# Performance work log

Hardware: AMD Instinct MI355X
Metric: run time of the kernel (lower is better)

## Reference

```python
import jax, jax.numpy as jnp
import numpy as np

N = 50000      # nodes
E = 800000     # edges (before self-loops)
IN = 128       # in_channels
C = 64         # hidden_channels
HD = 4         # heads
SLOPE = 0.2    # GATConv leaky_relu negative slope
EPS_BN = 1e-5


def add_self_loops(edge_index, n):
    loop = jnp.arange(n, dtype=edge_index.dtype)
    return jnp.concatenate([edge_index, jnp.stack([loop, loop])], axis=1)


def gat_conv(x, edge_index, W, a_src, a_dst, bias, heads, out_c, concat, n):
    src, dst = edge_index[0], edge_index[1]
    h = (x @ W).reshape(n, heads, out_c)                 # [N,H,C]
    al_s = jnp.sum(h * a_src, axis=-1)                   # [N,H]
    al_d = jnp.sum(h * a_dst, axis=-1)                   # [N,H]
    e = jax.nn.leaky_relu(al_s[src] + al_d[dst], SLOPE)  # [Etot,H]
    m = jax.ops.segment_max(e, dst, num_segments=n)      # segment softmax (stable)
    ex = jnp.exp(e - m[dst])
    s = jax.ops.segment_sum(ex, dst, num_segments=n)
    alpha = ex / (s[dst] + 1e-16)                        # [Etot,H]
    out = jax.ops.segment_sum(h[src] * alpha[:, :, None], dst, num_segments=n)
    out = out.reshape(n, heads * out_c) if concat else out.mean(axis=1)
    return out + bias


def batch_norm(x, gamma, beta):
    mu = x.mean(axis=0)
    var = x.var(axis=0)
    return (x - mu) * jax.lax.rsqrt(var + EPS_BN) * gamma + beta


def setup_inputs() -> dict:
    key = jax.random.key(0)
    ks = jax.random.split(key, 24)
    f = lambda k, shp, sc: (jax.random.normal(k, shp, dtype=jnp.float32) * sc)
    HC = HD * C
    return {
        "x": f(ks[0], (N, IN), 1.0),
        "edge_index": jax.random.randint(ks[1], (2, E), 0, N, dtype=jnp.int64),
        # conv1: IN -> C, heads=HD, concat
        "W1": f(ks[2], (IN, HC), 0.05), "as1": f(ks[3], (HD, C), 0.05),
        "ad1": f(ks[4], (HD, C), 0.05), "b1": f(ks[5], (HC,), 0.02),
        "g1": jnp.ones((HC,), jnp.float32), "bb1": jnp.zeros((HC,), jnp.float32),
        # conv2: HC -> C, heads=HD, concat
        "W2": f(ks[6], (HC, HC), 0.05), "as2": f(ks[7], (HD, C), 0.05),
        "ad2": f(ks[8], (HD, C), 0.05), "b2": f(ks[9], (HC,), 0.02),
        "g2": jnp.ones((HC,), jnp.float32), "bb2": jnp.zeros((HC,), jnp.float32),
        # conv3: HC -> C, heads=1, mean
        "W3": f(ks[10], (HC, C), 0.05), "as3": f(ks[11], (1, C), 0.05),
        "ad3": f(ks[12], (1, C), 0.05), "b3": f(ks[13], (C,), 0.02),
        # skips
        "Ws1": f(ks[14], (IN, HC), 0.05), "bs1": f(ks[15], (HC,), 0.02),
        "Ws2": f(ks[16], (HC, C), 0.05), "bs2": f(ks[17], (C,), 0.02),
    }


def reference(x, edge_index, W1, as1, ad1, b1, g1, bb1,
              W2, as2, ad2, b2, g2, bb2,
              W3, as3, ad3, b3, Ws1, bs1, Ws2, bs2):
    ei = add_self_loops(edge_index, N)
    x_init = x @ Ws1 + bs1
    h = gat_conv(x, ei, W1, as1, ad1, b1, HD, C, True, N)
    h = jax.nn.elu(batch_norm(h, g1, bb1)) + x_init
    x_skip = h @ Ws2 + bs2
    h = gat_conv(h, ei, W2, as2, ad2, b2, HD, C, True, N)
    h = jax.nn.elu(batch_norm(h, g2, bb2))
    out = gat_conv(h, ei, W3, as3, ad3, b3, 1, C, False, N) + x_skip
    return out
```

## Files before the change

kernel.cpp:

```cpp
#include <hip/hip_runtime.h>
#include <hip/hip_bf16.h>
#include <cstdint>
#include <cstddef>


#define LRELU_SLOPE 0.2f
#define NSTATB 256

typedef __attribute__((ext_vector_type(8))) short short8;
typedef __attribute__((ext_vector_type(4))) float f32x4;

__device__ __forceinline__ float bf2f(unsigned short u) {
  union { unsigned int i; float f; } t; t.i = ((unsigned int)u) << 16; return t.f;
}
__device__ __forceinline__ unsigned short f2bf(float f) {
  __hip_bfloat16 h = __float2bfloat16(f);
  return *reinterpret_cast<unsigned short*>(&h);
}

template<int K, int WAVES_GAT, int WAVES_SKIP>
__global__ __launch_bounds__((WAVES_GAT + WAVES_SKIP) * 64)
void gemm_gat_fused(const unsigned short* __restrict__ A,
                    const unsigned short* __restrict__ BtH,
                    const unsigned short* __restrict__ BtS,
                    const float* __restrict__ a_s, const float* __restrict__ a_d,
                    const float* __restrict__ biasS,
                    unsigned short* __restrict__ Hout,
                    float* __restrict__ als, float* __restrict__ ald,
                    unsigned short* __restrict__ Sout, int M) {
  constexpr int NKS = K / 32;
  constexpr int NH  = WAVES_GAT * 64;
  constexpr int NS  = WAVES_SKIP * 64;
  const int wid  = threadIdx.x >> 6;
  const int lane = threadIdx.x & 63;
  const int r    = lane & 15;
  const int q    = lane >> 4;
  const int koff = q * 8;
  const bool isGat = wid < WAVES_GAT;
  const int colbase = isGat ? wid * 64 : (wid - WAVES_GAT) * 64;
  const unsigned short* Bt = isGat ? BtH : BtS;

  short8 b[4][NKS];
  #pragma unroll
  for (int nf = 0; nf < 4; ++nf)
    #pragma unroll
    for (int ks = 0; ks < NKS; ++ks)
      b[nf][ks] = *(const short8*)(Bt + (size_t)(colbase + nf * 16 + r) * K + ks * 32 + koff);

  float as4[4] = {}, ad4[4] = {};
  if (isGat) {
    #pragma unroll
    for (int nf = 0; nf < 4; ++nf) {
      as4[nf] = a_s[colbase + nf * 16 + r];
      ad4[nf] = a_d[colbase + nf * 16 + r];
    }
  }

  const int ntiles = (M + 15) >> 4;
  const int chunk = (ntiles + 7) >> 3;
  const int xcd   = blockIdx.x & 7;
  const int lo    = xcd * chunk;
  const int hi    = min(lo + chunk, ntiles);
  const int bstep = gridDim.x >> 3;
  for (int t = lo + (blockIdx.x >> 3); t < hi; t += bstep) {
    const int row = t * 16 + r;
    short8 a[NKS];
    #pragma unroll
    for (int ks = 0; ks < NKS; ++ks) {
      a[ks] = (short8)(short)0;
      if (row < M) a[ks] = *(const short8*)(A + (size_t)row * K + ks * 32 + koff);
    }
    f32x4 acc[4];
    #pragma unroll
    for (int nf = 0; nf < 4; ++nf) acc[nf] = (f32x4)0.0f;
    #pragma unroll
    for (int ks = 0; ks < NKS; ++ks)
      #pragma unroll
      for (int nf = 0; nf < 4; ++nf)
        acc[nf] = __builtin_amdgcn_mfma_f32_16x16x32_bf16(a[ks], b[nf][ks], acc[nf], 0, 0, 0);

    const int rbase = t * 16 + q * 4;
    if (isGat) {
      #pragma unroll
      for (int nf = 0; nf < 4; ++nf) {
        const int col = colbase + nf * 16 + r;
        #pragma unroll
        for (int i = 0; i < 4; ++i) {
          const int rr = rbase + i;
          if (rr < M) Hout[(size_t)rr * NH + col] = f2bf(acc[nf][i]);
        }
      }
      #pragma unroll
      for (int i = 0; i < 4; ++i) {
        float s = 0.f, d = 0.f;
        #pragma unroll
        for (int nf = 0; nf < 4; ++nf) {
          s = fmaf(acc[nf][i], as4[nf], s);
          d = fmaf(acc[nf][i], ad4[nf], d);
        }
        #pragma unroll
        for (int m = 8; m >= 1; m >>= 1) {
          s += __shfl_xor(s, m, 64);
          d += __shfl_xor(d, m, 64);
        }
        const int rr = rbase + i;
        if (r == 0 && rr < M) {
          als[(size_t)rr * WAVES_GAT + wid] = s;
          ald[(size_t)rr * WAVES_GAT + wid] = d;
        }
      }
    } else {
      #pragma unroll
      for (int nf = 0; nf < 4; ++nf) {
        const int col = colbase + nf * 16 + r;
        const float bs = biasS[col];
        #pragma unroll
        for (int i = 0; i < 4; ++i) {
          const int rr = rbase + i;
          if (rr < M) Sout[(size_t)rr * NS + col] = f2bf(acc[nf][i] + bs);
        }
      }
    }
  }
}

__global__ __launch_bounds__(256)
void gemm_gat3(const unsigned short* __restrict__ A, const unsigned short* __restrict__ Bt,
               const float* __restrict__ a_s, const float* __restrict__ a_d,
               unsigned short* __restrict__ Hout, float* __restrict__ als,
               float* __restrict__ ald, int M) {
  constexpr int K = 256, NKS = 8;
  const int wid  = threadIdx.x >> 6;
  const int lane = threadIdx.x & 63;
  const int r    = lane & 15;
  const int q    = lane >> 4;
  const int koff = q * 8;

  short8 b[4][NKS];
  #pragma unroll
  for (int nf = 0; nf < 4; ++nf)
    #pragma unroll
    for (int ks = 0; ks < NKS; ++ks)
      b[nf][ks] = *(const short8*)(Bt + (size_t)(nf * 16 + r) * K + ks * 32 + koff);
  float as4[4], ad4[4];
  #pragma unroll
  for (int nf = 0; nf < 4; ++nf) {
    as4[nf] = a_s[nf * 16 + r];
    ad4[nf] = a_d[nf * 16 + r];
  }

  const int ntiles = (M + 15) >> 4;
  const int chunk = (ntiles + 7) >> 3;
  const int xcd   = blockIdx.x & 7;
  const int lo    = xcd * chunk;
  const int hi    = min(lo + chunk, ntiles);
  const int bstep = (gridDim.x >> 3) * 4;
  for (int t = lo + (blockIdx.x >> 3) * 4 + wid; t < hi; t += bstep) {
    const int row = t * 16 + r;
    short8 a[NKS];
    #pragma unroll
    for (int ks = 0; ks < NKS; ++ks) {
      a[ks] = (short8)(short)0;
      if (row < M) a[ks] = *(const short8*)(A + (size_t)row * K + ks * 32 + koff);
    }
    f32x4 acc[4];
    #pragma unroll
    for (int nf = 0; nf < 4; ++nf) acc[nf] = (f32x4)0.0f;
    #pragma unroll
    for (int ks = 0; ks < NKS; ++ks)
      #pragma unroll
      for (int nf = 0; nf < 4; ++nf)
        acc[nf] = __builtin_amdgcn_mfma_f32_16x16x32_bf16(a[ks], b[nf][ks], acc[nf], 0, 0, 0);

    const int rbase = t * 16 + q * 4;
    #pragma unroll
    for (int nf = 0; nf < 4; ++nf) {
      const int col = nf * 16 + r;
      #pragma unroll
      for (int i = 0; i < 4; ++i) {
        const int rr = rbase + i;
        if (rr < M) Hout[(size_t)rr * 64 + col] = f2bf(acc[nf][i]);
      }
    }
    #pragma unroll
    for (int i = 0; i < 4; ++i) {
      float s = 0.f, d = 0.f;
      #pragma unroll
      for (int nf = 0; nf < 4; ++nf) {
        s = fmaf(acc[nf][i], as4[nf], s);
        d = fmaf(acc[nf][i], ad4[nf], d);
      }
      #pragma unroll
      for (int m = 8; m >= 1; m >>= 1) {
        s += __shfl_xor(s, m, 64);
        d += __shfl_xor(d, m, 64);
      }
      const int rr = rbase + i;
      if (r == 0 && rr < M) { als[rr] = s; ald[rr] = d; }
    }
  }
}

__global__ __launch_bounds__(256)
void prep_all(const float* __restrict__ x,
              const float* __restrict__ W1, const float* __restrict__ Ws1,
              const float* __restrict__ W2, const float* __restrict__ Ws2,
              const float* __restrict__ W3,
              unsigned short* __restrict__ xb,
              unsigned short* __restrict__ W1t, unsigned short* __restrict__ Ws1t,
              unsigned short* __restrict__ W2t, unsigned short* __restrict__ Ws2t,
              unsigned short* __restrict__ W3t,
              int* __restrict__ cnt, int n) {
  int idx = blockIdx.x * blockDim.x + threadIdx.x;
  const int nx = n * 32;
  if (idx < nx) {
    float4 v = ((const float4*)x)[idx];
    ushort4 o;
    o.x = f2bf(v.x); o.y = f2bf(v.y); o.z = f2bf(v.z); o.w = f2bf(v.w);
    ((ushort4*)xb)[idx] = o;
    return;
  }
  idx -= nx;
  if (idx < 256 * 128) { int nn = idx >> 7, kk = idx & 127; W1t[idx]  = f2bf(W1[kk * 256 + nn]);  return; }
  idx -= 256 * 128;
  if (idx < 256 * 128) { int nn = idx >> 7, kk = idx & 127; Ws1t[idx] = f2bf(Ws1[kk * 256 + nn]); return; }
  idx -= 256 * 128;
  if (idx < 256 * 256) { int nn = idx >> 8, kk = idx & 255; W2t[idx]  = f2bf(W2[kk * 256 + nn]);  return; }
  idx -= 256 * 256;
  if (idx < 64 * 256)  { int nn = idx >> 8, kk = idx & 255; Ws2t[idx] = f2bf(Ws2[kk * 64 + nn]);  return; }
  idx -= 64 * 256;
  if (idx < 64 * 256)  { int nn = idx >> 8, kk = idx & 255; W3t[idx]  = f2bf(W3[kk * 64 + nn]); return; }
  idx -= 64 * 256;
  if (idx < n) cnt[idx] = 0;
}

__global__ void count_edges(const int* __restrict__ ei, int E, int* __restrict__ counts,
                            int n) {
  const int g = blockIdx.x & 7;
  const int chunk = (n + 7) >> 3;
  const int lo = g * chunk, hi = min(lo + chunk, n);
  const int stride = (gridDim.x >> 3) * blockDim.x;
  for (int i = (blockIdx.x >> 3) * blockDim.x + threadIdx.x; i < E; i += stride) {
    int d = ei[E + i];
    if (d >= lo && d < hi) atomicAdd(&counts[d], 1);
  }
}
__global__ void scan_block(const int* __restrict__ in, int* __restrict__ out,
                           int* __restrict__ bsums, int n) {
  __shared__ int tmp[256];
  int t = threadIdx.x;
  int gid = blockIdx.x * 256 + t;
  int v = (gid < n) ? in[gid] : 0;
  tmp[t] = v;
  __syncthreads();
  #pragma unroll
  for (int off = 1; off < 256; off <<= 1) {
    int x = (t >= off) ? tmp[t - off] : 0;
    __syncthreads();
    tmp[t] += x;
    __syncthreads();
  }
  if (gid < n) out[gid] = tmp[t] - v;
  if (t == 255) bsums[blockIdx.x] = tmp[255];
}
__global__ void scan_tops(const int* __restrict__ bsums, int* __restrict__ boffs, int nb) {
  __shared__ int tmp[256];
  int t = threadIdx.x;
  int v = (t < nb) ? bsums[t] : 0;
  tmp[t] = v;
  __syncthreads();
  #pragma unroll
  for (int off = 1; off < 256; off <<= 1) {
    int x = (t >= off) ? tmp[t - off] : 0;
    __syncthreads();
    tmp[t] += x;
    __syncthreads();
  }
  if (t < nb) boffs[t] = tmp[t] - v;
}
__global__ void scan_add(int* __restrict__ rp, const int* __restrict__ boffs,
                         int* __restrict__ cnt, int n, int etot) {
  int gid = blockIdx.x * 256 + threadIdx.x;
  if (gid < n) {
    rp[gid] += boffs[blockIdx.x];
    cnt[gid] = 0;
  }
  if (gid == 0) rp[n] = etot;
}
__global__ void fill_edges(const int* __restrict__ ei, int E, const int* __restrict__ rp,
                           int* __restrict__ cursor, int* __restrict__ csr, int n) {
  const int g = blockIdx.x & 7;
  const int chunk = (n + 7) >> 3;
  const int lo = g * chunk, hi = min(lo + chunk, n);
  const int stride = (gridDim.x >> 3) * blockDim.x;
  for (int i = (blockIdx.x >> 3) * blockDim.x + threadIdx.x; i < E; i += stride) {
    int d = ei[E + i];
    if (d >= lo && d < hi) {
      int pos = rp[d] + atomicAdd(&cursor[d], 1);
      csr[pos] = ei[i];
    }
  }
}

template<int HEADS, int HCt, bool OUT_BF16>
__global__ __launch_bounds__(256)
void gat_aggregate(const unsigned short* __restrict__ H, const float* __restrict__ als,
                   const float* __restrict__ ald, const int* __restrict__ rp,
                   const int* __restrict__ csr, const float* __restrict__ bias,
                   const unsigned short* __restrict__ skip, void* __restrict__ out, int n) {
  constexpr int CPL = HCt / 64;
  int w = (blockIdx.x * blockDim.x + threadIdx.x) >> 6;
  int lane = threadIdx.x & 63;
  if (w >= n) return;
  const int beg = rp[w], end = rp[w + 1];
  const int myhead = (HEADS == 1) ? 0 : (lane >> 4);
  const float adh = ald[(size_t)w * HEADS + myhead];

  auto att = [&](int s) -> float {
    float e = als[(size_t)s * HEADS + myhead] + adh;
    e = fmaxf(e, LRELU_SLOPE * e);
    return __expf(e);
  };

  float acc[CPL];
  float ssum = att(w);
  {
    const unsigned short* hp = H + (size_t)w * HCt + lane * CPL;
    if constexpr (CPL == 4) {
      ushort4 hv = *(const ushort4*)hp;
      acc[0] = ssum * bf2f(hv.x); acc[1] = ssum * bf2f(hv.y);
      acc[2] = ssum * bf2f(hv.z); acc[3] = ssum * bf2f(hv.w);
    } else {
      acc[0] = ssum * bf2f(hp[0]);
    }
  }

  int j = beg;
  for (; j + 8 <= end; j += 8) {
    int sidx[8];
    #pragma unroll
    for (int u = 0; u < 8; ++u) sidx[u] = csr[j + u];
    if constexpr (CPL == 4) {
      ushort4 hv[8];
      #pragma unroll
      for (int u = 0; u < 8; ++u)
        hv[u] = *(const ushort4*)(H + (size_t)sidx[u] * HCt + lane * 4);
      float ex[8];
      #pragma unroll
      for (int u = 0; u < 8; ++u) ex[u] = att(sidx[u]);
      #pragma unroll
      for (int u = 0; u < 8; ++u) {
        ssum += ex[u];
        acc[0] = fmaf(ex[u], bf2f(hv[u].x), acc[0]);
        acc[1] = fmaf(ex[u], bf2f(hv[u].y), acc[1]);
        acc[2] = fmaf(ex[u], bf2f(hv[u].z), acc[2]);
        acc[3] = fmaf(ex[u], bf2f(hv[u].w), acc[3]);
      }
    } else {
      unsigned short hv[8];
      #pragma unroll
      for (int u = 0; u < 8; ++u) hv[u] = H[(size_t)sidx[u] * HCt + lane];
      float ex[8];
      #pragma unroll
      for (int u = 0; u < 8; ++u) ex[u] = att(sidx[u]);
      #pragma unroll
      for (int u = 0; u < 8; ++u) {
        ssum += ex[u];
        acc[0] = fmaf(ex[u], bf2f(hv[u]), acc[0]);
      }
    }
  }
  for (; j + 4 <= end; j += 4) {
    int sidx[4];
    #pragma unroll
    for (int u = 0; u < 4; ++u) sidx[u] = csr[j + u];
    float ex[4];
    #pragma unroll
    for (int u = 0; u < 4; ++u) ex[u] = att(sidx[u]);
    if constexpr (CPL == 4) {
      ushort4 hv[4];
      #pragma unroll
      for (int u = 0; u < 4; ++u)
        hv[u] = *(const ushort4*)(H + (size_t)sidx[u] * HCt + lane * 4);
      #pragma unroll
      for (int u = 0; u < 4; ++u) {
        ssum += ex[u];
        acc[0] = fmaf(ex[u], bf2f(hv[u].x), acc[0]);
        acc[1] = fmaf(ex[u], bf2f(hv[u].y), acc[1]);
        acc[2] = fmaf(ex[u], bf2f(hv[u].z), acc[2]);
        acc[3] = fmaf(ex[u], bf2f(hv[u].w), acc[3]);
      }
    } else {
      unsigned short hv[4];
      #pragma unroll
      for (int u = 0; u < 4; ++u) hv[u] = H[(size_t)sidx[u] * HCt + lane];
      #pragma unroll
      for (int u = 0; u < 4; ++u) {
        ssum += ex[u];
        acc[0] = fmaf(ex[u], bf2f(hv[u]), acc[0]);
      }
    }
  }
  for (; j < end; ++j) {
    const int s = csr[j];
    const float ex = att(s);
    ssum += ex;
    const unsigned short* hp = H + (size_t)s * HCt + lane * CPL;
    if constexpr (CPL == 4) {
      ushort4 hv = *(const ushort4*)hp;
      acc[0] = fmaf(ex, bf2f(hv.x), acc[0]);
      acc[1] = fmaf(ex, bf2f(hv.y), acc[1]);
      acc[2] = fmaf(ex, bf2f(hv.z), acc[2]);
      acc[3] = fmaf(ex, bf2f(hv.w), acc[3]);
    } else {
      acc[0] = fmaf(ex, bf2f(hp[0]), acc[0]);
    }
  }

  const float inv = 1.f / (ssum + 1e-16f);
  #pragma unroll
  for (int c = 0; c < CPL; ++c) {
    int ch = lane * CPL + c;
    float v = acc[c] * inv + bias[ch];
    if (skip) v += bf2f(skip[(size_t)w * HCt + ch]);
    if constexpr (OUT_BF16)
      ((unsigned short*)out)[(size_t)w * HCt + ch] = f2bf(v);
    else
      ((float*)out)[(size_t)w * HCt + ch] = v;
  }
}

__global__ __launch_bounds__(256)
void bn_stats(const unsigned short* __restrict__ X, float* __restrict__ partial, int n) {
  const int lane = threadIdx.x & 63;
  const int rg   = threadIdx.x >> 6;
  const int c4   = lane * 4;
  float s0 = 0.f, s1 = 0.f, s2 = 0.f, s3 = 0.f;
  float q0 = 0.f, q1 = 0.f, q2 = 0.f, q3 = 0.f;
  const int step = NSTATB * 4;
  int r = blockIdx.x * 4 + rg;
  for (; r + 3 * step < n; r += 4 * step) {
    #pragma unroll
    for (int u = 0; u < 4; ++u) {
      ushort4 v = *(const ushort4*)(X + (size_t)(r + u * step) * 256 + c4);
      float f0 = bf2f(v.x), f1 = bf2f(v.y), f2 = bf2f(v.z), f3 = bf2f(v.w);
      s0 += f0; s1 += f1; s2 += f2; s3 += f3;
      q0 = fmaf(f0, f0, q0); q1 = fmaf(f1, f1, q1);
      q2 = fmaf(f2, f2, q2); q3 = fmaf(f3, f3, q3);
    }
  }
  for (; r < n; r += step) {
    ushort4 v = *(const ushort4*)(X + (size_t)r * 256 + c4);
    float f0 = bf2f(v.x), f1 = bf2f(v.y), f2 = bf2f(v.z), f3 = bf2f(v.w);
    s0 += f0; s1 += f1; s2 += f2; s3 += f3;
    q0 = fmaf(f0, f0, q0); q1 = fmaf(f1, f1, q1);
    q2 = fmaf(f2, f2, q2); q3 = fmaf(f3, f3, q3);
  }
  __shared__ float red[512];
  red[threadIdx.x] = 0.f;
  red[256 + threadIdx.x] = 0.f;
  __syncthreads();
  atomicAdd(&red[c4 + 0], s0); atomicAdd(&red[c4 + 1], s1);
  atomicAdd(&red[c4 + 2], s2); atomicAdd(&red[c4 + 3], s3);
  atomicAdd(&red[256 + c4 + 0], q0); atomicAdd(&red[256 + c4 + 1], q1);
  atomicAdd(&red[256 + c4 + 2], q2); atomicAdd(&red[256 + c4 + 3], q3);
  __syncthreads();
  partial[(size_t)blockIdx.x * 512 + threadIdx.x] = red[threadIdx.x];
  partial[(size_t)blockIdx.x * 512 + 256 + threadIdx.x] = red[256 + threadIdx.x];
}
__global__ __launch_bounds__(512)
void bn_finalize(const float* __restrict__ partial, const float* __restrict__ gamma,
                 const float* __restrict__ beta, float* __restrict__ scsh, int n) {
  __shared__ float sq[512];
  const int t = threadIdx.x;
  float acc = 0.f;
  #pragma unroll 8
  for (int r = 0; r < NSTATB; ++r) acc += partial[(size_t)r * 512 + t];
  sq[t] = acc;
  __syncthreads();
  if (t < 256) {
    float mean = sq[t] / (float)n;
    float var = sq[256 + t] / (float)n - mean * mean;
    float sc = gamma[t] * rsqrtf(var + 1e-5f);
    scsh[t] = sc;
    scsh[256 + t] = beta[t] - mean * sc;
  }
}
__global__ __launch_bounds__(256)
void bn_apply_elu(const unsigned short* __restrict__ X, const float* __restrict__ scsh,
                  const unsigned short* __restrict__ skip, unsigned short* __restrict__ Y,
                  int total) {
  int i4 = blockIdx.x * blockDim.x + threadIdx.x;
  if (i4 * 4 >= total) return;
  ushort4 xv = ((const ushort4*)X)[i4];
  int cb = (i4 * 4) & 255;
  float4 sc = *(const float4*)(scsh + cb);
  float4 sh = *(const float4*)(scsh + 256 + cb);
  float4 y;
  y.x = fmaf(bf2f(xv.x), sc.x, sh.x);
  y.y = fmaf(bf2f(xv.y), sc.y, sh.y);
  y.z = fmaf(bf2f(xv.z), sc.z, sh.z);
  y.w = fmaf(bf2f(xv.w), sc.w, sh.w);
  y.x = (y.x > 0.f) ? y.x : expm1f(y.x);
  y.y = (y.y > 0.f) ? y.y : expm1f(y.y);
  y.z = (y.z > 0.f) ? y.z : expm1f(y.z);
  y.w = (y.w > 0.f) ? y.w : expm1f(y.w);
  if (skip) {
    ushort4 s4 = ((const ushort4*)skip)[i4];
    y.x += bf2f(s4.x); y.y += bf2f(s4.y); y.z += bf2f(s4.z); y.w += bf2f(s4.w);
  }
  ushort4 o;
  o.x = f2bf(y.x); o.y = f2bf(y.y); o.z = f2bf(y.z); o.w = f2bf(y.w);
  ((ushort4*)Y)[i4] = o;
}

extern "C" void kernel_launch(void* const* d_in, const int* in_sizes, int n_in,
                              void* d_out, int out_size, void* d_ws, size_t ws_size,
                              hipStream_t stream) {
  const float* x   = (const float*)d_in[0];
  const int*   ei  = (const int*)d_in[1];
  const float* W1  = (const float*)d_in[2];
  const float* as1 = (const float*)d_in[3];
  const float* ad1 = (const float*)d_in[4];
  const float* b1  = (const float*)d_in[5];
  const float* g1  = (const float*)d_in[6];
  const float* bb1 = (const float*)d_in[7];
  const float* W2  = (const float*)d_in[8];
  const float* as2 = (const float*)d_in[9];
  const float* ad2 = (const float*)d_in[10];
  const float* b2  = (const float*)d_in[11];
  const float* g2  = (const float*)d_in[12];
  const float* bb2 = (const float*)d_in[13];
  const float* W3  = (const float*)d_in[14];
  const float* as3 = (const float*)d_in[15];
  const float* ad3 = (const float*)d_in[16];
  const float* b3  = (const float*)d_in[17];
  const float* Ws1 = (const float*)d_in[18];
  const float* bs1 = (const float*)d_in[19];
  const float* Ws2 = (const float*)d_in[20];
  const float* bs2 = (const float*)d_in[21];

  const int n = in_sizes[0] / 128;
  const int E = in_sizes[1] / 2;

  char* wsp = (char*)d_ws;
  auto carve = [&](size_t bytes) -> void* {
    void* p = (void*)wsp;
    wsp += (bytes + 255) & ~(size_t)255;
    return p;
  };
  unsigned short* Hb  = (unsigned short*)carve((size_t)n * 256 * 2);
  unsigned short* hb  = (unsigned short*)carve((size_t)n * 256 * 2);
  unsigned short* xbD = (unsigned short*)carve((size_t)n * 128 * 2);
  unsigned short* xb  = xbD;
  unsigned short* D   = xbD;
  unsigned short* Bv  = (unsigned short*)carve((size_t)n * 256 * 2);
  unsigned short* Cv  = (unsigned short*)carve((size_t)n * 256 * 2);
  float* als  = (float*)carve((size_t)n * 4 * 4);
  float* ald  = (float*)carve((size_t)n * 4 * 4);
  int*   rp   = (int*)carve((size_t)(n + 1) * 4);
  int*   cnt  = (int*)carve((size_t)n * 4);
  int*   bsums= (int*)carve(256 * 4);
  int*   boffs= (int*)carve(256 * 4);
  int*   csr  = (int*)carve((size_t)E * 4);
  float* partial = (float*)carve((size_t)NSTATB * 512 * 4);
  float* scsh = (float*)carve(512 * 4);
  unsigned short* W1t  = (unsigned short*)carve(128 * 256 * 2);
  unsigned short* Ws1t = (unsigned short*)carve(128 * 256 * 2);
  unsigned short* W2t  = (unsigned short*)carve(256 * 256 * 2);
  unsigned short* Ws2t = (unsigned short*)carve(256 * 64 * 2);
  unsigned short* W3t  = (unsigned short*)carve(256 * 64 * 2);

  const int NB = (n + 255) / 256;

  {
    const int total = n * 32 + 2 * 256 * 128 + 256 * 256 + 2 * 64 * 256 + n;
    prep_all<<<(total + 255) / 256, 256, 0, stream>>>(x, W1, Ws1, W2, Ws2, W3,
                                                      xb, W1t, Ws1t, W2t, Ws2t, W3t,
                                                      cnt, n);
  }

  count_edges<<<2048, 256, 0, stream>>>(ei, E, cnt, n);
  scan_block<<<NB, 256, 0, stream>>>(cnt, rp, bsums, n);
  scan_tops<<<1, 256, 0, stream>>>(bsums, boffs, NB);
  scan_add<<<NB, 256, 0, stream>>>(rp, boffs, cnt, n, E);
  fill_edges<<<2048, 256, 0, stream>>>(ei, E, rp, cnt, csr, n);

  const int wgrid = (n * 64 + 255) / 256;
  const int egrid = (n * 256 / 4 + 255) / 256;

  gemm_gat_fused<128, 4, 4><<<512, 512, 0, stream>>>(
      xb, W1t, Ws1t, as1, ad1, bs1, Hb, als, ald, Bv, n);
  gat_aggregate<4, 256, true><<<wgrid, 256, 0, stream>>>(Hb, als, ald, rp, csr, b1,
                                                         nullptr, Cv, n);
  bn_stats<<<NSTATB, 256, 0, stream>>>(Cv, partial, n);
  bn_finalize<<<1, 512, 0, stream>>>(partial, g1, bb1, scsh, n);
  bn_apply_elu<<<egrid, 256, 0, stream>>>(Cv, scsh, Bv, hb, n * 256);

  gemm_gat_fused<256, 4, 1><<<512, 320, 0, stream>>>(
      hb, W2t, Ws2t, as2, ad2, bs2, Hb, als, ald, D, n);
  gat_aggregate<4, 256, true><<<wgrid, 256, 0, stream>>>(Hb, als, ald, rp, csr, b2,
                                                         nullptr, Cv, n);
  bn_stats<<<NSTATB, 256, 0, stream>>>(Cv, partial, n);
  bn_finalize<<<1, 512, 0, stream>>>(partial, g2, bb2, scsh, n);
  bn_apply_elu<<<egrid, 256, 0, stream>>>(Cv, scsh, nullptr, hb, n * 256);

  gemm_gat3<<<512, 256, 0, stream>>>(hb, W3t, as3, ad3, Hb, als, ald, n);
  gat_aggregate<1, 64, false><<<wgrid, 256, 0, stream>>>(Hb, als, ald, rp, csr, b3, D,
                                                         d_out, n);
}
```

Before: 442.2 us.

## Merge scan kernels, scalarize CSR indices, widen BN apply, double GEMM grids

```diff
diff --git a/kernel.cpp b/kernel.cpp
--- a/kernel.cpp
+++ b/kernel.cpp
@@ -263,26 +263,18 @@
   if (gid < n) out[gid] = tmp[t] - v;
   if (t == 255) bsums[blockIdx.x] = tmp[255];
 }
-__global__ void scan_tops(const int* __restrict__ bsums, int* __restrict__ boffs, int nb) {
-  __shared__ int tmp[256];
-  int t = threadIdx.x;
-  int v = (t < nb) ? bsums[t] : 0;
-  tmp[t] = v;
+__global__ void scan_add(int* __restrict__ rp, const int* __restrict__ bsums,
+                         int* __restrict__ cnt, int n, int etot) {
+  __shared__ int boff;
+  if (threadIdx.x == 0) {
+    int s = 0;
+    for (int b = 0; b < (int)blockIdx.x; ++b) s += bsums[b];
+    boff = s;
+  }
   __syncthreads();
-  #pragma unroll
-  for (int off = 1; off < 256; off <<= 1) {
-    int x = (t >= off) ? tmp[t - off] : 0;
-    __syncthreads();
-    tmp[t] += x;
-    __syncthreads();
-  }
-  if (t < nb) boffs[t] = tmp[t] - v;
-}
-__global__ void scan_add(int* __restrict__ rp, const int* __restrict__ boffs,
-                         int* __restrict__ cnt, int n, int etot) {
   int gid = blockIdx.x * 256 + threadIdx.x;
   if (gid < n) {
-    rp[gid] += boffs[blockIdx.x];
+    rp[gid] += boff;
     cnt[gid] = 0;
   }
   if (gid == 0) rp[n] = etot;
@@ -339,7 +331,8 @@
   for (; j + 8 <= end; j += 8) {
     int sidx[8];
     #pragma unroll
-    for (int u = 0; u < 8; ++u) sidx[u] = csr[j + u];
+    for (int u = 0; u < 8; ++u)
+      sidx[u] = __builtin_amdgcn_readfirstlane(csr[j + u]);
     if constexpr (CPL == 4) {
       ushort4 hv[8];
       #pragma unroll
@@ -373,7 +366,8 @@
   for (; j + 4 <= end; j += 4) {
     int sidx[4];
     #pragma unroll
-    for (int u = 0; u < 4; ++u) sidx[u] = csr[j + u];
+    for (int u = 0; u < 4; ++u)
+      sidx[u] = __builtin_amdgcn_readfirstlane(csr[j + u]);
     float ex[4];
     #pragma unroll
     for (int u = 0; u < 4; ++u) ex[u] = att(sidx[u]);
@@ -402,7 +396,7 @@
     }
   }
   for (; j < end; ++j) {
-    const int s = csr[j];
+    const int s = __builtin_amdgcn_readfirstlane(csr[j]);
     const float ex = att(s);
     ssum += ex;
     const unsigned short* hp = H + (size_t)s * HCt + lane * CPL;
@@ -490,28 +484,19 @@
 void bn_apply_elu(const unsigned short* __restrict__ X, const float* __restrict__ scsh,
                   const unsigned short* __restrict__ skip, unsigned short* __restrict__ Y,
                   int total) {
-  int i4 = blockIdx.x * blockDim.x + threadIdx.x;
-  if (i4 * 4 >= total) return;
-  ushort4 xv = ((const ushort4*)X)[i4];
-  int cb = (i4 * 4) & 255;
-  float4 sc = *(const float4*)(scsh + cb);
-  float4 sh = *(const float4*)(scsh + 256 + cb);
-  float4 y;
-  y.x = fmaf(bf2f(xv.x), sc.x, sh.x);
-  y.y = fmaf(bf2f(xv.y), sc.y, sh.y);
-  y.z = fmaf(bf2f(xv.z), sc.z, sh.z);
-  y.w = fmaf(bf2f(xv.w), sc.w, sh.w);
-  y.x = (y.x > 0.f) ? y.x : expm1f(y.x);
-  y.y = (y.y > 0.f) ? y.y : expm1f(y.y);
-  y.z = (y.z > 0.f) ? y.z : expm1f(y.z);
-  y.w = (y.w > 0.f) ? y.w : expm1f(y.w);
-  if (skip) {
-    ushort4 s4 = ((const ushort4*)skip)[i4];
-    y.x += bf2f(s4.x); y.y += bf2f(s4.y); y.z += bf2f(s4.z); y.w += bf2f(s4.w);
-  }
-  ushort4 o;
-  o.x = f2bf(y.x); o.y = f2bf(y.y); o.z = f2bf(y.z); o.w = f2bf(y.w);
-  ((ushort4*)Y)[i4] = o;
+  int i8 = blockIdx.x * blockDim.x + threadIdx.x;
+  if (i8 * 8 >= total) return;
+  short8 xv = ((const short8*)X)[i8];
+  int cb = (i8 * 8) & 255;
+  short8 o;
+  #pragma unroll
+  for (int u = 0; u < 8; ++u) {
+    float yv = fmaf(bf2f((unsigned short)xv[u]), scsh[cb + u], scsh[256 + cb + u]);
+    yv = (yv > 0.f) ? yv : expm1f(yv);
+    if (skip) yv += bf2f(((const unsigned short*)skip)[(size_t)i8 * 8 + u]);
+    o[u] = (short)f2bf(yv);
+  }
+  ((short8*)Y)[i8] = o;
 }
 
 extern "C" void kernel_launch(void* const* d_in, const int* in_sizes, int n_in,
@@ -561,7 +546,6 @@
   int*   rp   = (int*)carve((size_t)(n + 1) * 4);
   int*   cnt  = (int*)carve((size_t)n * 4);
   int*   bsums= (int*)carve(256 * 4);
-  int*   boffs= (int*)carve(256 * 4);
   int*   csr  = (int*)carve((size_t)E * 4);
   float* partial = (float*)carve((size_t)NSTATB * 512 * 4);
   float* scsh = (float*)carve(512 * 4);
@@ -582,30 +566,29 @@
 
   count_edges<<<2048, 256, 0, stream>>>(ei, E, cnt, n);
   scan_block<<<NB, 256, 0, stream>>>(cnt, rp, bsums, n);
-  scan_tops<<<1, 256, 0, stream>>>(bsums, boffs, NB);
-  scan_add<<<NB, 256, 0, stream>>>(rp, boffs, cnt, n, E);
+  scan_add<<<NB, 256, 0, stream>>>(rp, bsums, cnt, n, E);
   fill_edges<<<2048, 256, 0, stream>>>(ei, E, rp, cnt, csr, n);
 
   const int wgrid = (n * 64 + 255) / 256;
-  const int egrid = (n * 256 / 4 + 255) / 256;
-
-  gemm_gat_fused<128, 4, 4><<<512, 512, 0, stream>>>(
+  const int e8grid = (n * 256 / 8 + 255) / 256;
+
+  gemm_gat_fused<128, 4, 4><<<1024, 512, 0, stream>>>(
       xb, W1t, Ws1t, as1, ad1, bs1, Hb, als, ald, Bv, n);
   gat_aggregate<4, 256, true><<<wgrid, 256, 0, stream>>>(Hb, als, ald, rp, csr, b1,
                                                          nullptr, Cv, n);
   bn_stats<<<NSTATB, 256, 0, stream>>>(Cv, partial, n);
   bn_finalize<<<1, 512, 0, stream>>>(partial, g1, bb1, scsh, n);
-  bn_apply_elu<<<egrid, 256, 0, stream>>>(Cv, scsh, Bv, hb, n * 256);
-
-  gemm_gat_fused<256, 4, 1><<<512, 320, 0, stream>>>(
+  bn_apply_elu<<<e8grid, 256, 0, stream>>>(Cv, scsh, Bv, hb, n * 256);
+
+  gemm_gat_fused<256, 4, 1><<<1024, 320, 0, stream>>>(
       hb, W2t, Ws2t, as2, ad2, bs2, Hb, als, ald, D, n);
   gat_aggregate<4, 256, true><<<wgrid, 256, 0, stream>>>(Hb, als, ald, rp, csr, b2,
                                                          nullptr, Cv, n);
   bn_stats<<<NSTATB, 256, 0, stream>>>(Cv, partial, n);
   bn_finalize<<<1, 512, 0, stream>>>(partial, g2, bb2, scsh, n);
-  bn_apply_elu<<<egrid, 256, 0, stream>>>(Cv, scsh, nullptr, hb, n * 256);
-
-  gemm_gat3<<<512, 256, 0, stream>>>(hb, W3t, as3, ad3, Hb, als, ald, n);
+  bn_apply_elu<<<e8grid, 256, 0, stream>>>(Cv, scsh, nullptr, hb, n * 256);
+
+  gemm_gat3<<<1024, 256, 0, stream>>>(hb, W3t, as3, ad3, Hb, als, ald, n);
   gat_aggregate<1, 64, false><<<wgrid, 256, 0, stream>>>(Hb, als, ald, rp, csr, b3, D,
                                                          d_out, n);
 }
```

Result: slower. 555.7 us (+25.7%).
